# Optimization experiments

Measured on AMD Instinct MI355X. Metric: run time of the kernel, lower is better.

## Reference

```python
import jax, jax.numpy as jnp
import numpy as np

B, C, H, W = 8, 256, 64, 64


def setup_inputs() -> dict:
    key = jax.random.key(0)
    ks = jax.random.split(key, 9)
    s = 1.0 / np.sqrt(C)  # conv2d default init scale
    return {
        "foreground": jax.random.normal(ks[0], (B, C, H, W), jnp.float32),
        "background": jax.random.normal(ks[1], (B, C, H, W), jnp.float32),
        "mask": jax.random.uniform(ks[2], (B, C, H, W), jnp.float32),
        "Wq": jax.random.normal(ks[3], (C, C), jnp.float32) * s,
        "bq": jnp.zeros((C,), jnp.float32),
        "Wk": jax.random.normal(ks[4], (C, C), jnp.float32) * s,
        "bk": jnp.zeros((C,), jnp.float32),
        "Wv": jax.random.normal(ks[5], (C, C), jnp.float32) * s,
        "bv": jnp.zeros((C,), jnp.float32),
        "gamma": jnp.ones((1,), jnp.float32),
    }


def _conv1x1(x, Wt, b):
    # 1x1 conv == per-pixel channel matmul; x: [B,C,H,W], Wt: [Cout,Cin]
    return jnp.einsum('bchw,oc->bohw', x, Wt) + b[None, :, None, None]


def reference(foreground, background, mask, Wq, bq, Wk, bk, Wv, bv, gamma):
    b, c, h, w = foreground.shape
    hw = h * w
    # mask is already at feature resolution (interpolate would be identity)
    q = _conv1x1(foreground, Wq, bq).reshape(b, c, hw)   # [B,C,HW]
    k = _conv1x1(background, Wk, bk).reshape(b, c, hw)   # [B,C,HW]
    # bmm(q, k^T): channel-channel correlation [B,C,C]
    corr = jnp.einsum('bci,bdi->bcd', q, k)
    m_r = mask.reshape(b, c, hw)                          # [B,C,HW]
    # bmm(corr, m_r): mask-modulated scores [B,C,HW]
    scores = jnp.einsum('bcd,bdi->bci', corr, m_r)
    energy = jax.nn.softmax(scores, axis=-1)
    v = _conv1x1(foreground, Wv, bv).reshape(b, c, hw)
    attended = (energy * v).reshape(b, c, h, w)
    out = foreground * mask + gamma[0] * (1.0 - mask) * attended
    return out
```

## Files before the change

kernel.cpp:

```cpp
#include <hip/hip_runtime.h>
#include <math.h>

#define B_    8
#define C_    256
#define HW_   4096
#define CHW_  ((long)C_ * HW_)

#define BKT   32
#define LDH   40
#define KS    16
#define KCH   (HW_ / KS)

typedef __attribute__((ext_vector_type(8))) short bf16x8;
typedef __attribute__((ext_vector_type(4))) float f32x4;
#define MFMA_BF16(a, b, c) __builtin_amdgcn_mfma_f32_16x16x32_bf16((a), (b), (c), 0, 0, 0)

__device__ __forceinline__ void cvt_hl4(const float4 f, uint* h, uint* l) {
    uint u0 = __float_as_uint(f.x), u1 = __float_as_uint(f.y),
         u2 = __float_as_uint(f.z), u3 = __float_as_uint(f.w);
    uint h0 = (u0 + 0x8000u) & 0xFFFF0000u, h1 = (u1 + 0x8000u) & 0xFFFF0000u,
         h2 = (u2 + 0x8000u) & 0xFFFF0000u, h3 = (u3 + 0x8000u) & 0xFFFF0000u;
    h[0] = (h0 >> 16) | h1;
    h[1] = (h2 >> 16) | h3;
    float l0 = f.x - __uint_as_float(h0), l1 = f.y - __uint_as_float(h1),
          l2 = f.z - __uint_as_float(h2), l3 = f.w - __uint_as_float(h3);
    uint a0 = __float_as_uint(l0) & 0xFFFF0000u, a1 = __float_as_uint(l1) & 0xFFFF0000u,
         a2 = __float_as_uint(l2) & 0xFFFF0000u, a3 = __float_as_uint(l3) & 0xFFFF0000u;
    l[0] = (a0 >> 16) | a1;
    l[1] = (a2 >> 16) | a3;
}
__device__ __forceinline__ void cvt_h4(const float4 f, uint* h) {
    uint u0 = __float_as_uint(f.x), u1 = __float_as_uint(f.y),
         u2 = __float_as_uint(f.z), u3 = __float_as_uint(f.w);
    uint h0 = (u0 + 0x8000u) & 0xFFFF0000u, h1 = (u1 + 0x8000u) & 0xFFFF0000u,
         h2 = (u2 + 0x8000u) & 0xFFFF0000u, h3 = (u3 + 0x8000u) & 0xFFFF0000u;
    h[0] = (h0 >> 16) | h1;
    h[1] = (h2 >> 16) | h3;
}

__global__ __launch_bounds__(256) void conv_w(
    const float* __restrict__ Wv, ushort* __restrict__ Wvh)
{
    const int i = (blockIdx.x * 256 + threadIdx.x) * 4;
    float4 v = *reinterpret_cast<const float4*>(&Wv[i]);
    uint h[2];
    cvt_h4(v, h);
    *reinterpret_cast<uint2*>(&Wvh[i]) = make_uint2(h[0], h[1]);
}

__global__ __launch_bounds__(256) void conv_transpose(
    const float* __restrict__ mask, const float* __restrict__ fg,
    ushort* __restrict__ mTh, ushort* __restrict__ mTl, ushort* __restrict__ fTh)
{
    __shared__ float tile[64][65];
    const int zi = blockIdx.z;
    const bool domask = zi < B_;
    const int b = domask ? zi : zi - B_;
    const float* src = (domask ? mask : fg) + (long)b * CHW_;
    const int e0 = blockIdx.y * 64, i0 = blockIdx.x * 64;

    const int t  = threadIdx.x;
    const int tr = t >> 4, tc = (t & 15) * 4;

    #pragma unroll
    for (int j = 0; j < 4; ++j) {
        const int e = tr + j * 16;
        float4 v = *reinterpret_cast<const float4*>(&src[(long)(e0 + e) * HW_ + i0 + tc]);
        tile[e][tc + 0] = v.x; tile[e][tc + 1] = v.y;
        tile[e][tc + 2] = v.z; tile[e][tc + 3] = v.w;
    }
    __syncthreads();

    #pragma unroll
    for (int j = 0; j < 4; ++j) {
        const int i = tr + j * 16;
        float4 v = make_float4(tile[tc + 0][i], tile[tc + 1][i], tile[tc + 2][i], tile[tc + 3][i]);
        const long o = (long)b * CHW_ + (long)(i0 + i) * C_ + e0 + tc;
        if (domask) {
            uint h[2], l[2];
            cvt_hl4(v, h, l);
            *reinterpret_cast<uint2*>(&mTh[o]) = make_uint2(h[0], h[1]);
            *reinterpret_cast<uint2*>(&mTl[o]) = make_uint2(l[0], l[1]);
        } else {
            uint h[2];
            cvt_h4(v, h);
            *reinterpret_cast<uint2*>(&fTh[o]) = make_uint2(h[0], h[1]);
        }
    }
}

__global__ __launch_bounds__(256, 3) void gemm_nt_mfma(
    const float* __restrict__ F, const float* __restrict__ G,
    float* __restrict__ part,
    float* __restrict__ fsum, float* __restrict__ gsum)
{
    __shared__ ushort Ah[128 * LDH], Al[128 * LDH], Bh[128 * LDH], Bl[128 * LDH];

    const int z  = blockIdx.z;
    const int b  = z >> 4;
    const int ks = z & (KS - 1);
    const int c0 = blockIdx.y * 128;
    const int d0 = blockIdx.x * 128;
    const float* Fb = F + (long)b * CHW_ + (long)ks * KCH;
    const float* Gb = G + (long)b * CHW_ + (long)ks * KCH;
    const bool doF = (blockIdx.x == 0);
    const bool doG = (blockIdx.y == 0);

    const int t    = threadIdx.x;
    const int srow = t >> 1;
    const int sk   = (t & 1) * 16;
    const int lane = t & 63, w = t >> 6;
    const int col  = lane & 15, quad = lane >> 4;
    const int wm   = (w >> 1) * 64, wn = (w & 1) * 64;

    f32x4 acc[4][4] = {};
    float rsF = 0.0f, rsG = 0.0f;

    for (int kt = 0; kt < KCH; kt += BKT) {
        {
            const float* s = &Fb[(long)(c0 + srow) * HW_ + kt + sk];
            float4 v0 = *reinterpret_cast<const float4*>(s);
            float4 v1 = *reinterpret_cast<const float4*>(s + 4);
            float4 v2 = *reinterpret_cast<const float4*>(s + 8);
            float4 v3 = *reinterpret_cast<const float4*>(s + 12);
            if (doF) {
                rsF += (v0.x + v0.y + v0.z + v0.w) + (v1.x + v1.y + v1.z + v1.w)
                     + (v2.x + v2.y + v2.z + v2.w) + (v3.x + v3.y + v3.z + v3.w);
            }
            uint h[4], l[4];
            cvt_hl4(v0, h + 0, l + 0);
            cvt_hl4(v1, h + 2, l + 2);
            *reinterpret_cast<uint4*>(&Ah[srow * LDH + sk]) = make_uint4(h[0], h[1], h[2], h[3]);
            *reinterpret_cast<uint4*>(&Al[srow * LDH + sk]) = make_uint4(l[0], l[1], l[2], l[3]);
            cvt_hl4(v2, h + 0, l + 0);
            cvt_hl4(v3, h + 2, l + 2);
            *reinterpret_cast<uint4*>(&Ah[srow * LDH + sk + 8]) = make_uint4(h[0], h[1], h[2], h[3]);
            *reinterpret_cast<uint4*>(&Al[srow * LDH + sk + 8]) = make_uint4(l[0], l[1], l[2], l[3]);
        }
        {
            const float* s = &Gb[(long)(d0 + srow) * HW_ + kt + sk];
            float4 v0 = *reinterpret_cast<const float4*>(s);
            float4 v1 = *reinterpret_cast<const float4*>(s + 4);
            float4 v2 = *reinterpret_cast<const float4*>(s + 8);
            float4 v3 = *reinterpret_cast<const float4*>(s + 12);
            if (doG) {
                rsG += (v0.x + v0.y + v0.z + v0.w) + (v1.x + v1.y + v1.z + v1.w)
                     + (v2.x + v2.y + v2.z + v2.w) + (v3.x + v3.y + v3.z + v3.w);
            }
            uint h[4], l[4];
            cvt_hl4(v0, h + 0, l + 0);
            cvt_hl4(v1, h + 2, l + 2);
            *reinterpret_cast<uint4*>(&Bh[srow * LDH + sk]) = make_uint4(h[0], h[1], h[2], h[3]);
            *reinterpret_cast<uint4*>(&Bl[srow * LDH + sk]) = make_uint4(l[0], l[1], l[2], l[3]);
            cvt_hl4(v2, h + 0, l + 0);
            cvt_hl4(v3, h + 2, l + 2);
            *reinterpret_cast<uint4*>(&Bh[srow * LDH + sk + 8]) = make_uint4(h[0], h[1], h[2], h[3]);
            *reinterpret_cast<uint4*>(&Bl[srow * LDH + sk + 8]) = make_uint4(l[0], l[1], l[2], l[3]);
        }
        __syncthreads();

        bf16x8 bfh[4], bfl[4];
        #pragma unroll
        for (int tj = 0; tj < 4; ++tj) {
            const int r = (wn + tj * 16 + col) * LDH + quad * 8;
            bfh[tj] = *reinterpret_cast<const bf16x8*>(&Bh[r]);
            bfl[tj] = *reinterpret_cast<const bf16x8*>(&Bl[r]);
        }
        #pragma unroll
        for (int ti = 0; ti < 4; ++ti) {
            const int r = (wm + ti * 16 + col) * LDH + quad * 8;
            bf16x8 afh = *reinterpret_cast<const bf16x8*>(&Ah[r]);
            bf16x8 afl = *reinterpret_cast<const bf16x8*>(&Al[r]);
            #pragma unroll
            for (int tj = 0; tj < 4; ++tj) {
                acc[ti][tj] = MFMA_BF16(afh, bfh[tj], acc[ti][tj]);
                acc[ti][tj] = MFMA_BF16(afh, bfl[tj], acc[ti][tj]);
                acc[ti][tj] = MFMA_BF16(afl, bfh[tj], acc[ti][tj]);
            }
        }
        __syncthreads();
    }

    rsF += __shfl_xor(rsF, 1);
    rsG += __shfl_xor(rsG, 1);
    if (doF && (t & 1) == 0) atomicAdd(&fsum[b * C_ + c0 + srow], rsF);
    if (doG && (t & 1) == 0) atomicAdd(&gsum[b * C_ + d0 + srow], rsG);

    float* P = part + (long)z * C_ * C_;
    #pragma unroll
    for (int ti = 0; ti < 4; ++ti) {
        const int m = c0 + wm + ti * 16 + quad * 4;
        #pragma unroll
        for (int tj = 0; tj < 4; ++tj) {
            const int n = d0 + wn + tj * 16 + col;
            #pragma unroll
            for (int r = 0; r < 4; ++r)
                P[(long)(m + r) * C_ + n] = acc[ti][tj][r];
        }
    }
}

__global__ __launch_bounds__(256, 3) void gemm_scores_mfma(
    const ushort* __restrict__ corrh, const ushort* __restrict__ corrl,
    const ushort* __restrict__ mTh,   const ushort* __restrict__ mTl,
    float* __restrict__ S, float* __restrict__ pmax, float* __restrict__ psum)
{
    __shared__ ushort Ah[128 * LDH], Al[128 * LDH], Bh[128 * LDH], Bl[128 * LDH];
    __shared__ float pm[2][128], ps[2][128];

    const int b  = blockIdx.z;
    const int m0 = blockIdx.y * 128;
    const int n0 = blockIdx.x * 128;
    const ushort* Ahb = corrh + (long)b * C_ * C_;
    const ushort* Alb = corrl + (long)b * C_ * C_;
    const ushort* Bhb = mTh + (long)b * CHW_;
    const ushort* Blb = mTl + (long)b * CHW_;

    const int t    = threadIdx.x;
    const int srow = t >> 1;
    const int sk   = (t & 1) * 16;
    const int lane = t & 63, w = t >> 6;
    const int col  = lane & 15, quad = lane >> 4;
    const int wm   = (w >> 1) * 64, wn = (w & 1) * 64;

    f32x4 acc[4][4] = {};

    for (int kt = 0; kt < C_; kt += BKT) {
        const long ga = (long)(m0 + srow) * C_ + kt + sk;
        const long gb = (long)(n0 + srow) * C_ + kt + sk;
        uint4 ah0 = *reinterpret_cast<const uint4*>(&Ahb[ga]);
        uint4 ah1 = *reinterpret_cast<const uint4*>(&Ahb[ga + 8]);
        uint4 al0 = *reinterpret_cast<const uint4*>(&Alb[ga]);
        uint4 al1 = *reinterpret_cast<const uint4*>(&Alb[ga + 8]);
        uint4 bh0 = *reinterpret_cast<const uint4*>(&Bhb[gb]);
        uint4 bh1 = *reinterpret_cast<const uint4*>(&Bhb[gb + 8]);
        uint4 bl0 = *reinterpret_cast<const uint4*>(&Blb[gb]);
        uint4 bl1 = *reinterpret_cast<const uint4*>(&Blb[gb + 8]);
        *reinterpret_cast<uint4*>(&Ah[srow * LDH + sk])     = ah0;
        *reinterpret_cast<uint4*>(&Ah[srow * LDH + sk + 8]) = ah1;
        *reinterpret_cast<uint4*>(&Al[srow * LDH + sk])     = al0;
        *reinterpret_cast<uint4*>(&Al[srow * LDH + sk + 8]) = al1;
        *reinterpret_cast<uint4*>(&Bh[srow * LDH + sk])     = bh0;
        *reinterpret_cast<uint4*>(&Bh[srow * LDH + sk + 8]) = bh1;
        *reinterpret_cast<uint4*>(&Bl[srow * LDH + sk])     = bl0;
        *reinterpret_cast<uint4*>(&Bl[srow * LDH + sk + 8]) = bl1;
        __syncthreads();

        bf16x8 bfh[4], bfl[4];
        #pragma unroll
        for (int tj = 0; tj < 4; ++tj) {
            const int r = (wn + tj * 16 + col) * LDH + quad * 8;
            bfh[tj] = *reinterpret_cast<const bf16x8*>(&Bh[r]);
            bfl[tj] = *reinterpret_cast<const bf16x8*>(&Bl[r]);
        }
        #pragma unroll
        for (int ti = 0; ti < 4; ++ti) {
            const int r = (wm + ti * 16 + col) * LDH + quad * 8;
            bf16x8 afh = *reinterpret_cast<const bf16x8*>(&Ah[r]);
            bf16x8 afl = *reinterpret_cast<const bf16x8*>(&Al[r]);
            #pragma unroll
            for (int tj = 0; tj < 4; ++tj) {
                acc[ti][tj] = MFMA_BF16(afh, bfh[tj], acc[ti][tj]);
                acc[ti][tj] = MFMA_BF16(afh, bfl[tj], acc[ti][tj]);
                acc[ti][tj] = MFMA_BF16(afl, bfh[tj], acc[ti][tj]);
            }
        }
        __syncthreads();
    }

    float* Sb = S + (long)b * CHW_;
    #pragma unroll
    for (int ti = 0; ti < 4; ++ti) {
        const int m = m0 + wm + ti * 16 + quad * 4;
        #pragma unroll
        for (int tj = 0; tj < 4; ++tj) {
            const int n = n0 + wn + tj * 16 + col;
            #pragma unroll
            for (int r = 0; r < 4; ++r)
                Sb[(long)(m + r) * HW_ + n] = acc[ti][tj][r];
        }
    }

    #pragma unroll
    for (int ti = 0; ti < 4; ++ti) {
        #pragma unroll
        for (int r = 0; r < 4; ++r) {
            float mx = fmaxf(fmaxf(acc[ti][0][r], acc[ti][1][r]),
                             fmaxf(acc[ti][2][r], acc[ti][3][r]));
            mx = fmaxf(mx, __shfl_xor(mx, 1));
            mx = fmaxf(mx, __shfl_xor(mx, 2));
            mx = fmaxf(mx, __shfl_xor(mx, 4));
            mx = fmaxf(mx, __shfl_xor(mx, 8));
            float se = __expf(acc[ti][0][r] - mx) + __expf(acc[ti][1][r] - mx)
                     + __expf(acc[ti][2][r] - mx) + __expf(acc[ti][3][r] - mx);
            se += __shfl_xor(se, 1);
            se += __shfl_xor(se, 2);
            se += __shfl_xor(se, 4);
            se += __shfl_xor(se, 8);
            if (col == 0) {
                const int rb = wm + ti * 16 + quad * 4 + r;
                pm[w & 1][rb] = mx;
                ps[w & 1][rb] = se;
            }
        }
    }
    __syncthreads();
    if (t < 128) {
        const float a0 = pm[0][t], a1 = pm[1][t];
        const float gm = fmaxf(a0, a1);
        const float gs = ps[0][t] * __expf(a0 - gm) + ps[1][t] * __expf(a1 - gm);
        const long rowg = (long)b * C_ + m0 + t;
        pmax[rowg * 32 + blockIdx.x] = gm;
        psum[rowg * 32 + blockIdx.x] = gs;
    }
}

__global__ __launch_bounds__(256) void combine_stats(
    const float* __restrict__ pmax, const float* __restrict__ psum,
    float* __restrict__ stats)
{
    const int row = blockIdx.x * 256 + threadIdx.x;
    const float* pmr = pmax + (long)row * 32;
    const float* psr = psum + (long)row * 32;
    float gm = -INFINITY;
    #pragma unroll
    for (int i = 0; i < 32; ++i) gm = fmaxf(gm, pmr[i]);
    float gs = 0.0f;
    #pragma unroll
    for (int i = 0; i < 32; ++i) gs += psr[i] * __expf(pmr[i] - gm);
    stats[row]        = gm;
    stats[2048 + row] = gs;
}

__global__ __launch_bounds__(256, 3) void gemm_v_final_mfma(
    const ushort* __restrict__ Wvh, const ushort* __restrict__ fTh,
    const float* __restrict__ bv, const float* __restrict__ fg,
    const float* __restrict__ mask, const float* __restrict__ S,
    const float* __restrict__ stats, const float* __restrict__ gamma,
    float* __restrict__ out)
{
    __shared__ ushort Ahh[128 * LDH], Bhh[128 * LDH];

    const int b  = blockIdx.z;
    const int m0 = blockIdx.y * 128;
    const int n0 = blockIdx.x * 128;
    const ushort* Bb = fTh + (long)b * CHW_;

    const int t    = threadIdx.x;
    const int srow = t >> 1;
    const int sk   = (t & 1) * 16;
    const int lane = t & 63, w = t >> 6;
    const int col  = lane & 15, quad = lane >> 4;
    const int wm   = (w >> 1) * 64, wn = (w & 1) * 64;

    f32x4 acc[4][4] = {};

    for (int kt = 0; kt < C_; kt += BKT) {
        const long ga = (long)(m0 + srow) * C_ + kt + sk;
        const long gb = (long)(n0 + srow) * C_ + kt + sk;
        uint4 a0 = *reinterpret_cast<const uint4*>(&Wvh[ga]);
        uint4 a1 = *reinterpret_cast<const uint4*>(&Wvh[ga + 8]);
        uint4 b0 = *reinterpret_cast<const uint4*>(&Bb[gb]);
        uint4 b1 = *reinterpret_cast<const uint4*>(&Bb[gb + 8]);
        *reinterpret_cast<uint4*>(&Ahh[srow * LDH + sk])     = a0;
        *reinterpret_cast<uint4*>(&Ahh[srow * LDH + sk + 8]) = a1;
        *reinterpret_cast<uint4*>(&Bhh[srow * LDH + sk])     = b0;
        *reinterpret_cast<uint4*>(&Bhh[srow * LDH + sk + 8]) = b1;
        __syncthreads();

        bf16x8 bfh[4];
        #pragma unroll
        for (int tj = 0; tj < 4; ++tj)
            bfh[tj] = *reinterpret_cast<const bf16x8*>(&Bhh[(wn + tj * 16 + col) * LDH + quad * 8]);
        #pragma unroll
        for (int ti = 0; ti < 4; ++ti) {
            bf16x8 afh = *reinterpret_cast<const bf16x8*>(&Ahh[(wm + ti * 16 + col) * LDH + quad * 8]);
            #pragma unroll
            for (int tj = 0; tj < 4; ++tj)
                acc[ti][tj] = MFMA_BF16(afh, bfh[tj], acc[ti][tj]);
        }
        __syncthreads();
    }

    const float g = gamma[0];
    #pragma unroll
    for (int ti = 0; ti < 4; ++ti) {
        const int m = m0 + wm + ti * 16 + quad * 4;
        #pragma unroll
        for (int r = 0; r < 4; ++r) {
            const int row  = b * C_ + m + r;
            const float mx  = stats[row];
            const float inv = 1.0f / stats[B_ * C_ + row];
            const float bvm = bv[m + r];
            #pragma unroll
            for (int tj = 0; tj < 4; ++tj) {
                const int n = n0 + wn + tj * 16 + col;
                const long e = (long)b * CHW_ + (long)(m + r) * HW_ + n;
                const float f  = fg[e];
                const float mk = mask[e];
                const float sv = S[e];
                const float vv = acc[ti][tj][r] + bvm;
                out[e] = f * mk + g * (1.0f - mk) * (__expf(sv - mx) * inv) * vv;
            }
        }
    }
}

__global__ __launch_bounds__(256) void reduce_part(
    const float* __restrict__ part, float* __restrict__ S1)
{
    const long idx = (long)blockIdx.x * 256 + threadIdx.x;
    const int  b   = (int)(idx >> 16);
    const long e   = idx & 65535;
    const float* p = part + ((long)b * KS) * 65536 + e;
    float s = 0.0f;
    #pragma unroll
    for (int ks = 0; ks < KS; ++ks) s += p[(long)ks * 65536];
    S1[idx] = s;
}

__global__ __launch_bounds__(256) void uvw_kernel(
    const float* __restrict__ Wq, const float* __restrict__ Wk,
    const float* __restrict__ bk,
    const float* __restrict__ fsum, const float* __restrict__ gsum,
    float* __restrict__ u, float* __restrict__ wh)
{
    const int g = blockIdx.x * 256 + threadIdx.x;
    if (g < 2048) {
        const int b = g >> 8, c = g & 255;
        const float* w = Wq + (long)c * C_;
        const float* s = fsum + b * C_;
        float acc = 0.0f;
        for (int e = 0; e < C_; ++e) acc = fmaf(w[e], s[e], acc);
        u[g] = acc;
    } else {
        const int g2 = g - 2048;
        const int b = g2 >> 8, d = g2 & 255;
        const float* w = Wk + (long)d * C_;
        const float* s = gsum + b * C_;
        float acc = 0.0f;
        for (int f = 0; f < C_; ++f) acc = fmaf(w[f], s[f], acc);
        wh[g2] = acc + (float)HW_ * bk[d];
    }
}

#define BK64 16
#define LDT64 68
__global__ __launch_bounds__(256) void gemm_nt64(
    const float* __restrict__ S1, const float* __restrict__ Wk,
    float* __restrict__ T)
{
    __shared__ float As[BK64][LDT64];
    __shared__ float Bs[BK64][LDT64];
    const int r0 = blockIdx.y * 64;
    const int d0 = blockIdx.x * 64;
    const int t   = threadIdx.x;
    const int tx  = t & 15, ty = t >> 4;
    const int tx4 = tx * 4, ty4 = ty * 4;
    const int am  = t >> 2, ak4 = (t & 3) * 4;

    float acc[4][4] = {};
    for (int k0 = 0; k0 < C_; k0 += BK64) {
        float4 av = *reinterpret_cast<const float4*>(&S1[(long)(r0 + am) * C_ + k0 + ak4]);
        float4 bw = *reinterpret_cast<const float4*>(&Wk[(long)(d0 + am) * C_ + k0 + ak4]);
        As[ak4+0][am]=av.x; As[ak4+1][am]=av.y; As[ak4+2][am]=av.z; As[ak4+3][am]=av.w;
        Bs[ak4+0][am]=bw.x; Bs[ak4+1][am]=bw.y; Bs[ak4+2][am]=bw.z; Bs[ak4+3][am]=bw.w;
        __syncthreads();
        #pragma unroll
        for (int kk = 0; kk < BK64; ++kk) {
            float4 a = *reinterpret_cast<const float4*>(&As[kk][ty4]);
            float4 x = *reinterpret_cast<const float4*>(&Bs[kk][tx4]);
            const float ar[4] = {a.x,a.y,a.z,a.w};
            const float xr[4] = {x.x,x.y,x.z,x.w};
            #pragma unroll
            for (int r = 0; r < 4; ++r)
                #pragma unroll
                for (int s = 0; s < 4; ++s)
                    acc[r][s] = fmaf(ar[r], xr[s], acc[r][s]);
        }
        __syncthreads();
    }
    #pragma unroll
    for (int r = 0; r < 4; ++r) {
        float4 o; o.x=acc[r][0]; o.y=acc[r][1]; o.z=acc[r][2]; o.w=acc[r][3];
        *reinterpret_cast<float4*>(&T[(long)(r0 + ty4 + r) * C_ + d0 + tx4]) = o;
    }
}

__global__ __launch_bounds__(256) void gemm_nn64_rank1(
    const float* __restrict__ Wq, const float* __restrict__ T,
    const float* __restrict__ u,  const float* __restrict__ bk,
    const float* __restrict__ bq, const float* __restrict__ wh,
    ushort* __restrict__ corrh, ushort* __restrict__ corrl)
{
    __shared__ float As[BK64][LDT64];
    __shared__ float Bs[BK64][LDT64];
    const int b  = blockIdx.z;
    const int m0 = blockIdx.y * 64;
    const int n0 = blockIdx.x * 64;
    const float* Tb = T + (long)b * C_ * C_;

    const int t   = threadIdx.x;
    const int tx  = t & 15, ty = t >> 4;
    const int tx4 = tx * 4, ty4 = ty * 4;
    const int am  = t >> 2, ak4 = (t & 3) * 4;
    const int xk  = ty,     xn4 = tx4;

    float acc[4][4] = {};
    for (int k0 = 0; k0 < C_; k0 += BK64) {
        float4 av = *reinterpret_cast<const float4*>(&Wq[(long)(m0 + am) * C_ + k0 + ak4]);
        float4 xv = *reinterpret_cast<const float4*>(&Tb[(long)(k0 + xk) * C_ + n0 + xn4]);
        As[ak4+0][am]=av.x; As[ak4+1][am]=av.y; As[ak4+2][am]=av.z; As[ak4+3][am]=av.w;
        *reinterpret_cast<float4*>(&Bs[xk][xn4]) = xv;
        __syncthreads();
        #pragma unroll
        for (int kk = 0; kk < BK64; ++kk) {
            float4 a = *reinterpret_cast<const float4*>(&As[kk][ty4]);
            float4 x = *reinterpret_cast<const float4*>(&Bs[kk][tx4]);
            const float ar[4] = {a.x,a.y,a.z,a.w};
            const float xr[4] = {x.x,x.y,x.z,x.w};
            #pragma unroll
            for (int r = 0; r < 4; ++r)
                #pragma unroll
                for (int s = 0; s < 4; ++s)
                    acc[r][s] = fmaf(ar[r], xr[s], acc[r][s]);
        }
        __syncthreads();
    }

    float4 bkv = *reinterpret_cast<const float4*>(&bk[n0 + tx4]);
    float4 whv = *reinterpret_cast<const float4*>(&wh[b * C_ + n0 + tx4]);
    #pragma unroll
    for (int r = 0; r < 4; ++r) {
        const int m = m0 + ty4 + r;
        const float um = u[b * C_ + m];
        const float bm = bq[m];
        float4 o;
        o.x = acc[r][0] + um*bkv.x + bm*whv.x;
        o.y = acc[r][1] + um*bkv.y + bm*whv.y;
        o.z = acc[r][2] + um*bkv.z + bm*whv.z;
        o.w = acc[r][3] + um*bkv.w + bm*whv.w;
        uint h[2], l[2];
        cvt_hl4(o, h, l);
        const long e = (long)b * C_ * C_ + (long)m * C_ + n0 + tx4;
        *reinterpret_cast<uint2*>(&corrh[e]) = make_uint2(h[0], h[1]);
        *reinterpret_cast<uint2*>(&corrl[e]) = make_uint2(l[0], l[1]);
    }
}

extern "C" void kernel_launch(void* const* d_in, const int* in_sizes, int n_in,
                              void* d_out, int out_size, void* d_ws, size_t ws_size,
                              hipStream_t stream)
{
    const float* fg    = (const float*)d_in[0];
    const float* bg    = (const float*)d_in[1];
    const float* mask  = (const float*)d_in[2];
    const float* Wq    = (const float*)d_in[3];
    const float* bq    = (const float*)d_in[4];
    const float* Wk    = (const float*)d_in[5];
    const float* bk    = (const float*)d_in[6];
    const float* Wv    = (const float*)d_in[7];
    const float* bv    = (const float*)d_in[8];
    const float* gamma = (const float*)d_in[9];
    float* out = (float*)d_out;

    char* ws = (char*)d_ws;
    float*  part   = (float*)(ws);
    float*  scores = (float*)(ws);
    ushort* mTh    = (ushort*)(ws + 33554432);
    ushort* mTl    = (ushort*)(ws + 50331648);
    ushort* fTh    = (ushort*)(ws + 67108864);
    float*  S1     = (float*)(ws + 83886080);
    float*  T      = (float*)(ws + 85983232);
    ushort* corrh  = (ushort*)(ws + 88080384);
    ushort* corrl  = (ushort*)(ws + 89128960);
    ushort* Wvh    = (ushort*)(ws + 90177536);
    float*  stats  = (float*)(ws + 90308608);
    float*  fsum   = (float*)(ws + 90324992);
    float*  gsum   = (float*)(ws + 90333184);
    float*  u      = (float*)(ws + 90341376);
    float*  wh     = (float*)(ws + 90349568);
    float*  pmax   = (float*)(ws + 90357760);
    float*  psum   = (float*)(ws + 90619904);

    const dim3 blk(256);

    hipMemsetAsync(fsum, 0, 16384, stream);

    conv_transpose<<<dim3(HW_ / 64, C_ / 64, 2 * B_), blk, 0, stream>>>(
        mask, fg, mTh, mTl, fTh);
    conv_w<<<dim3(64), blk, 0, stream>>>(Wv, Wvh);

    gemm_nt_mfma<<<dim3(2, 2, B_ * KS), blk, 0, stream>>>(fg, bg, part, fsum, gsum);
    reduce_part<<<dim3(B_ * C_ * C_ / 256), blk, 0, stream>>>(part, S1);

    uvw_kernel<<<dim3(16), blk, 0, stream>>>(Wq, Wk, bk, fsum, gsum, u, wh);

    gemm_nt64<<<dim3(C_ / 64, B_ * C_ / 64), blk, 0, stream>>>(S1, Wk, T);
    gemm_nn64_rank1<<<dim3(4, 4, B_), blk, 0, stream>>>(Wq, T, u, bk, bq, wh, corrh, corrl);

    gemm_scores_mfma<<<dim3(HW_ / 128, C_ / 128, B_), blk, 0, stream>>>(
        corrh, corrl, mTh, mTl, scores, pmax, psum);
    combine_stats<<<dim3(8), blk, 0, stream>>>(pmax, psum, stats);

    gemm_v_final_mfma<<<dim3(HW_ / 128, C_ / 128, B_), blk, 0, stream>>>(
        Wvh, fTh, bv, fg, mask, scores, stats, gamma, out);
}
```

Before: 284.0 us.

## Recompute scores in final kernel instead of storing them, fuse stats combine

The scores GEMM now emits only per-tile softmax max/sum partials and no longer writes the full B×C×HW score tensor. The final kernel recomputes the scores tile with a split-bf16 MFMA GEMM, folds the stats-combine step in per block, and then computes the V projection and output. This removes a 32 MB write and read of scores plus one kernel launch, at the cost of running the three-pass scores GEMM twice and using smaller 128x64 output tiles in the final kernel.

```diff
diff --git a/kernel.cpp b/kernel.cpp
--- a/kernel.cpp
+++ b/kernel.cpp
@@ -200,10 +200,10 @@
     }
 }
 
-__global__ __launch_bounds__(256, 3) void gemm_scores_mfma(
+__global__ __launch_bounds__(256, 3) void gemm_stats_mfma(
     const ushort* __restrict__ corrh, const ushort* __restrict__ corrl,
     const ushort* __restrict__ mTh,   const ushort* __restrict__ mTl,
-    float* __restrict__ S, float* __restrict__ pmax, float* __restrict__ psum)
+    float* __restrict__ pmax, float* __restrict__ psum)
 {
     __shared__ ushort Ah[128 * LDH], Al[128 * LDH], Bh[128 * LDH], Bl[128 * LDH];
     __shared__ float pm[2][128], ps[2][128];
@@ -268,19 +268,6 @@
         __syncthreads();
     }
 
-    float* Sb = S + (long)b * CHW_;
-    #pragma unroll
-    for (int ti = 0; ti < 4; ++ti) {
-        const int m = m0 + wm + ti * 16 + quad * 4;
-        #pragma unroll
-        for (int tj = 0; tj < 4; ++tj) {
-            const int n = n0 + wn + tj * 16 + col;
-            #pragma unroll
-            for (int r = 0; r < 4; ++r)
-                Sb[(long)(m + r) * HW_ + n] = acc[ti][tj][r];
-        }
-    }
-
     #pragma unroll
     for (int ti = 0; ti < 4; ++ti) {
         #pragma unroll
@@ -315,92 +302,146 @@
     }
 }
 
-__global__ __launch_bounds__(256) void combine_stats(
-    const float* __restrict__ pmax, const float* __restrict__ psum,
-    float* __restrict__ stats)
-{
-    const int row = blockIdx.x * 256 + threadIdx.x;
-    const float* pmr = pmax + (long)row * 32;
-    const float* psr = psum + (long)row * 32;
-    float gm = -INFINITY;
-    #pragma unroll
-    for (int i = 0; i < 32; ++i) gm = fmaxf(gm, pmr[i]);
-    float gs = 0.0f;
-    #pragma unroll
-    for (int i = 0; i < 32; ++i) gs += psr[i] * __expf(pmr[i] - gm);
-    stats[row]        = gm;
-    stats[2048 + row] = gs;
-}
-
-__global__ __launch_bounds__(256, 3) void gemm_v_final_mfma(
-    const ushort* __restrict__ Wvh, const ushort* __restrict__ fTh,
-    const float* __restrict__ bv, const float* __restrict__ fg,
-    const float* __restrict__ mask, const float* __restrict__ S,
-    const float* __restrict__ stats, const float* __restrict__ gamma,
+__global__ __launch_bounds__(256, 3) void gemm_fused_final(
+    const ushort* __restrict__ corrh, const ushort* __restrict__ corrl,
+    const ushort* __restrict__ mTh,   const ushort* __restrict__ mTl,
+    const ushort* __restrict__ Wvh,   const ushort* __restrict__ fTh,
+    const float* __restrict__ pmax,   const float* __restrict__ psum,
+    const float* __restrict__ bv,     const float* __restrict__ fg,
+    const float* __restrict__ mask,   const float* __restrict__ gamma,
     float* __restrict__ out)
 {
-    __shared__ ushort Ahh[128 * LDH], Bhh[128 * LDH];
+    __shared__ ushort Ah[128 * LDH], Al[128 * LDH];
+    __shared__ ushort Bh[64 * LDH],  Bl[64 * LDH];
+    __shared__ float sm[128], si[128];
 
     const int b  = blockIdx.z;
     const int m0 = blockIdx.y * 128;
-    const int n0 = blockIdx.x * 128;
-    const ushort* Bb = fTh + (long)b * CHW_;
-
-    const int t    = threadIdx.x;
-    const int srow = t >> 1;
-    const int sk   = (t & 1) * 16;
-    const int lane = t & 63, w = t >> 6;
-    const int col  = lane & 15, quad = lane >> 4;
-    const int wm   = (w >> 1) * 64, wn = (w & 1) * 64;
-
-    f32x4 acc[4][4] = {};
-
+    const int n0 = blockIdx.x * 64;
+    const ushort* Ahb = corrh + (long)b * C_ * C_;
+    const ushort* Alb = corrl + (long)b * C_ * C_;
+    const ushort* Bhb = mTh + (long)b * CHW_;
+    const ushort* Blb = mTl + (long)b * CHW_;
+    const ushort* Fb  = fTh + (long)b * CHW_;
+
+    const int t     = threadIdx.x;
+    const int srow  = t >> 1;
+    const int sk    = (t & 1) * 16;
+    const int srowB = t >> 2;
+    const int skB   = (t & 3) * 8;
+    const int lane  = t & 63, w = t >> 6;
+    const int col   = lane & 15, quad = lane >> 4;
+    const int wm    = (w >> 1) * 64, wn = (w & 1) * 32;
+
+    if (t < 128) {
+        const long rowg = (long)b * C_ + m0 + t;
+        const float* pmr = pmax + rowg * 32;
+        const float* psr = psum + rowg * 32;
+        float gm = -INFINITY;
+        #pragma unroll
+        for (int i = 0; i < 32; ++i) gm = fmaxf(gm, pmr[i]);
+        float gs = 0.0f;
+        #pragma unroll
+        for (int i = 0; i < 32; ++i) gs += psr[i] * __expf(pmr[i] - gm);
+        sm[t] = gm;
+        si[t] = 1.0f / gs;
+    }
+
+    f32x4 acc_s[4][2] = {};
     for (int kt = 0; kt < C_; kt += BKT) {
         const long ga = (long)(m0 + srow) * C_ + kt + sk;
-        const long gb = (long)(n0 + srow) * C_ + kt + sk;
+        const long gb = (long)(n0 + srowB) * C_ + kt + skB;
+        uint4 ah0 = *reinterpret_cast<const uint4*>(&Ahb[ga]);
+        uint4 ah1 = *reinterpret_cast<const uint4*>(&Ahb[ga + 8]);
+        uint4 al0 = *reinterpret_cast<const uint4*>(&Alb[ga]);
+        uint4 al1 = *reinterpret_cast<const uint4*>(&Alb[ga + 8]);
+        uint4 bh0 = *reinterpret_cast<const uint4*>(&Bhb[gb]);
+        uint4 bl0 = *reinterpret_cast<const uint4*>(&Blb[gb]);
+        __syncthreads();
+        *reinterpret_cast<uint4*>(&Ah[srow * LDH + sk])     = ah0;
+        *reinterpret_cast<uint4*>(&Ah[srow * LDH + sk + 8]) = ah1;
+        *reinterpret_cast<uint4*>(&Al[srow * LDH + sk])     = al0;
+        *reinterpret_cast<uint4*>(&Al[srow * LDH + sk + 8]) = al1;
+        *reinterpret_cast<uint4*>(&Bh[srowB * LDH + skB])   = bh0;
+        *reinterpret_cast<uint4*>(&Bl[srowB * LDH + skB])   = bl0;
+        __syncthreads();
+
+        bf16x8 bfh[2], bfl[2];
+        #pragma unroll
+        for (int tj = 0; tj < 2; ++tj) {
+            const int r = (wn + tj * 16 + col) * LDH + quad * 8;
+            bfh[tj] = *reinterpret_cast<const bf16x8*>(&Bh[r]);
+            bfl[tj] = *reinterpret_cast<const bf16x8*>(&Bl[r]);
+        }
+        #pragma unroll
+        for (int ti = 0; ti < 4; ++ti) {
+            const int r = (wm + ti * 16 + col) * LDH + quad * 8;
+            bf16x8 afh = *reinterpret_cast<const bf16x8*>(&Ah[r]);
+            bf16x8 afl = *reinterpret_cast<const bf16x8*>(&Al[r]);
+            #pragma unroll
+            for (int tj = 0; tj < 2; ++tj) {
+                acc_s[ti][tj] = MFMA_BF16(afh, bfh[tj], acc_s[ti][tj]);
+                acc_s[ti][tj] = MFMA_BF16(afh, bfl[tj], acc_s[ti][tj]);
+                acc_s[ti][tj] = MFMA_BF16(afl, bfh[tj], acc_s[ti][tj]);
+            }
+        }
+    }
+    __syncthreads();
+
+    const float g = gamma[0];
+    #pragma unroll
+    for (int ti = 0; ti < 4; ++ti) {
+        #pragma unroll
+        for (int r = 0; r < 4; ++r) {
+            const int lrow = wm + ti * 16 + quad * 4 + r;
+            const float mx  = sm[lrow];
+            const float inv = si[lrow] * g;
+            #pragma unroll
+            for (int tj = 0; tj < 2; ++tj)
+                acc_s[ti][tj][r] = __expf(acc_s[ti][tj][r] - mx) * inv;
+        }
+    }
+
+    f32x4 acc_v[4][2] = {};
+    for (int kt = 0; kt < C_; kt += BKT) {
+        const long ga = (long)(m0 + srow) * C_ + kt + sk;
+        const long gb = (long)(n0 + srowB) * C_ + kt + skB;
         uint4 a0 = *reinterpret_cast<const uint4*>(&Wvh[ga]);
         uint4 a1 = *reinterpret_cast<const uint4*>(&Wvh[ga + 8]);
-        uint4 b0 = *reinterpret_cast<const uint4*>(&Bb[gb]);
-        uint4 b1 = *reinterpret_cast<const uint4*>(&Bb[gb + 8]);
-        *reinterpret_cast<uint4*>(&Ahh[srow * LDH + sk])     = a0;
-        *reinterpret_cast<uint4*>(&Ahh[srow * LDH + sk + 8]) = a1;
-        *reinterpret_cast<uint4*>(&Bhh[srow * LDH + sk])     = b0;
-        *reinterpret_cast<uint4*>(&Bhh[srow * LDH + sk + 8]) = b1;
-        __syncthreads();
-
-        bf16x8 bfh[4];
-        #pragma unroll
-        for (int tj = 0; tj < 4; ++tj)
-            bfh[tj] = *reinterpret_cast<const bf16x8*>(&Bhh[(wn + tj * 16 + col) * LDH + quad * 8]);
+        uint4 b0 = *reinterpret_cast<const uint4*>(&Fb[gb]);
+        __syncthreads();
+        *reinterpret_cast<uint4*>(&Ah[srow * LDH + sk])     = a0;
+        *reinterpret_cast<uint4*>(&Ah[srow * LDH + sk + 8]) = a1;
+        *reinterpret_cast<uint4*>(&Bh[srowB * LDH + skB])   = b0;
+        __syncthreads();
+
+        bf16x8 bfh[2];
+        #pragma unroll
+        for (int tj = 0; tj < 2; ++tj)
+            bfh[tj] = *reinterpret_cast<const bf16x8*>(&Bh[(wn + tj * 16 + col) * LDH + quad * 8]);
         #pragma unroll
         for (int ti = 0; ti < 4; ++ti) {
-            bf16x8 afh = *reinterpret_cast<const bf16x8*>(&Ahh[(wm + ti * 16 + col) * LDH + quad * 8]);
-            #pragma unroll
-            for (int tj = 0; tj < 4; ++tj)
-                acc[ti][tj] = MFMA_BF16(afh, bfh[tj], acc[ti][tj]);
-        }
-        __syncthreads();
-    }
-
-    const float g = gamma[0];
+            bf16x8 afh = *reinterpret_cast<const bf16x8*>(&Ah[(wm + ti * 16 + col) * LDH + quad * 8]);
+            #pragma unroll
+            for (int tj = 0; tj < 2; ++tj)
+                acc_v[ti][tj] = MFMA_BF16(afh, bfh[tj], acc_v[ti][tj]);
+        }
+    }
+
     #pragma unroll
     for (int ti = 0; ti < 4; ++ti) {
         const int m = m0 + wm + ti * 16 + quad * 4;
         #pragma unroll
         for (int r = 0; r < 4; ++r) {
-            const int row  = b * C_ + m + r;
-            const float mx  = stats[row];
-            const float inv = 1.0f / stats[B_ * C_ + row];
             const float bvm = bv[m + r];
             #pragma unroll
-            for (int tj = 0; tj < 4; ++tj) {
+            for (int tj = 0; tj < 2; ++tj) {
                 const int n = n0 + wn + tj * 16 + col;
                 const long e = (long)b * CHW_ + (long)(m + r) * HW_ + n;
                 const float f  = fg[e];
                 const float mk = mask[e];
-                const float sv = S[e];
-                const float vv = acc[ti][tj][r] + bvm;
-                out[e] = f * mk + g * (1.0f - mk) * (__expf(sv - mx) * inv) * vv;
+                const float vv = acc_v[ti][tj][r] + bvm;
+                out[e] = f * mk + (1.0f - mk) * acc_s[ti][tj][r] * vv;
             }
         }
     }
@@ -566,7 +607,6 @@
 
     char* ws = (char*)d_ws;
     float*  part   = (float*)(ws);
-    float*  scores = (float*)(ws);
     ushort* mTh    = (ushort*)(ws + 33554432);
     ushort* mTl    = (ushort*)(ws + 50331648);
     ushort* fTh    = (ushort*)(ws + 67108864);
@@ -575,13 +615,12 @@
     ushort* corrh  = (ushort*)(ws + 88080384);
     ushort* corrl  = (ushort*)(ws + 89128960);
     ushort* Wvh    = (ushort*)(ws + 90177536);
-    float*  stats  = (float*)(ws + 90308608);
-    float*  fsum   = (float*)(ws + 90324992);
-    float*  gsum   = (float*)(ws + 90333184);
-    float*  u      = (float*)(ws + 90341376);
-    float*  wh     = (float*)(ws + 90349568);
-    float*  pmax   = (float*)(ws + 90357760);
-    float*  psum   = (float*)(ws + 90619904);
+    float*  fsum   = (float*)(ws + 90308608);
+    float*  gsum   = (float*)(ws + 90316800);
+    float*  u      = (float*)(ws + 90324992);
+    float*  wh     = (float*)(ws + 90333184);
+    float*  pmax   = (float*)(ws + 90341376);
+    float*  psum   = (float*)(ws + 90603520);
 
     const dim3 blk(256);
 
@@ -599,10 +638,9 @@
     gemm_nt64<<<dim3(C_ / 64, B_ * C_ / 64), blk, 0, stream>>>(S1, Wk, T);
     gemm_nn64_rank1<<<dim3(4, 4, B_), blk, 0, stream>>>(Wq, T, u, bk, bq, wh, corrh, corrl);
 
-    gemm_scores_mfma<<<dim3(HW_ / 128, C_ / 128, B_), blk, 0, stream>>>(
-        corrh, corrl, mTh, mTl, scores, pmax, psum);
-    combine_stats<<<dim3(8), blk, 0, stream>>>(pmax, psum, stats);
-
-    gemm_v_final_mfma<<<dim3(HW_ / 128, C_ / 128, B_), blk, 0, stream>>>(
-        Wvh, fTh, bv, fg, mask, scores, stats, gamma, out);
-}
+    gemm_stats_mfma<<<dim3(HW_ / 128, C_ / 128, B_), blk, 0, stream>>>(
+        corrh, corrl, mTh, mTl, pmax, psum);
+
+    gemm_fused_final<<<dim3(HW_ / 64, C_ / 128, B_), blk, 0, stream>>>(
+        corrh, corrl, mTh, mTl, Wvh, fTh, pmax, psum, bv, fg, mask, gamma, out);
+}
```

After: 286.3 us. Within noise of the previous version (+0.8%).
